# Performance work log

Hardware: AMD Instinct MI355X
Metric: run time of the kernel (lower is better)

## Reference

```python
import jax, jax.numpy as jnp
import numpy as np

B, N, C = 8, 1024, 1024
H = 16
D = C // H  # head_dim = 64


def apply_rope(t, cos, sin):
    # t: (B,H,N,D), cos/sin: (N, D//2). Interleaved-pair RoPE
    # (matches repeat_interleave(2) + stack(-y2,y1) in the torch code).
    tr = t.reshape(*t.shape[:-1], D // 2, 2)
    t1, t2 = tr[..., 0], tr[..., 1]
    o1 = t1 * cos - t2 * sin
    o2 = t2 * cos + t1 * sin
    return jnp.stack((o1, o2), axis=-1).reshape(t.shape)


def setup_inputs() -> dict:
    key = jax.random.key(0)
    k1, k2, k3, k4 = jax.random.split(key, 4)
    s = 0.02
    x = jax.random.normal(k1, (B, N, C), dtype=jnp.float32)
    w_qkv = jax.random.normal(k2, (C, 3 * C), dtype=jnp.float32) * s  # qkv_bias=False
    w_proj = jax.random.normal(k3, (C, C), dtype=jnp.float32) * s
    b_proj = jax.random.normal(k4, (C,), dtype=jnp.float32) * s
    return {"x": x, "w_qkv": w_qkv, "w_proj": w_proj, "b_proj": b_proj}


def reference(x, w_qkv, w_proj, b_proj):
    # QKV projection: (B,N,3C) -> (3,B,H,N,D)
    qkv = (x @ w_qkv).reshape(B, N, 3, H, D).transpose(2, 0, 3, 1, 4)
    q, k, v = qkv[0], qkv[1], qkv[2]

    # RoPE tables: pos = arange(N) (mask=None, no cls/registers)
    pos = jnp.arange(N, dtype=jnp.float32)
    omega = 1.0 / (10000.0 ** (jnp.arange(D // 2, dtype=jnp.float32) / (D / 2.0)))
    freq = pos[:, None] * omega  # (N, D//2)
    cos, sin = jnp.cos(freq), jnp.sin(freq)

    q = apply_rope(q, cos, sin)
    k = apply_rope(k, cos, sin)

    # Scaled dot-product attention (non-causal, no dropout in eval)
    scale = 1.0 / jnp.sqrt(jnp.float32(D))
    scores = jnp.einsum('bhqd,bhkd->bhqk', q, k) * scale
    attn = jax.nn.softmax(scores, axis=-1)
    out = jnp.einsum('bhqk,bhkd->bhqd', attn, v)

    # Merge heads + output projection
    out = out.transpose(0, 2, 1, 3).reshape(B, N, C)
    return out @ w_proj + b_proj
```

## Files before the change

kernel.cpp:

```cpp
#include <hip/hip_runtime.h>
#include <hip/hip_bf16.h>
#include <math.h>

#define Bsz  8
#define Nseq 1024
#define Cdim 1024
#define Hh   16
#define Dd   64

typedef short short8 __attribute__((ext_vector_type(8)));
typedef float floatx4 __attribute__((ext_vector_type(4)));

__device__ __forceinline__ unsigned short f2bf(float f) {
    __hip_bfloat16 h = __float2bfloat16(f);
    return __builtin_bit_cast(unsigned short, h);
}

__device__ __forceinline__ void async16(const void* g, void* l) {
    __builtin_amdgcn_global_load_lds(
        (const __attribute__((address_space(1))) unsigned int*)g,
        (__attribute__((address_space(3))) unsigned int*)l, 16, 0, 0);
}

__device__ __forceinline__ unsigned pack_bf16(float lo, float hi) {
    unsigned ulo = __float_as_uint(lo) + 0x8000u;
    unsigned uhi = __float_as_uint(hi) + 0x8000u;
    return __builtin_amdgcn_perm(uhi, ulo, 0x07060302);
}

__global__ __launch_bounds__(256) void prep(
    const float* __restrict__ x, const float* __restrict__ w_qkv,
    const float* __restrict__ w_proj,
    unsigned short* __restrict__ xb, unsigned short* __restrict__ wqkvt,
    unsigned short* __restrict__ wprojt, float2* __restrict__ rope)
{
    __shared__ float T[64][65];
    const int blk = blockIdx.x;
    const int tid = threadIdx.x;

    if (blk < 8192) {
        int i = blk * 256 + tid;
        float4 v = ((const float4*)x)[i];
        ushort4 u;
        u.x = f2bf(v.x); u.y = f2bf(v.y); u.z = f2bf(v.z); u.w = f2bf(v.w);
        ((ushort4*)xb)[i] = u;
        return;
    }
    if (blk < 9216) {
        const float* in;
        unsigned short* out;
        int R = 1024, Ccols, c0, r0;
        if (blk < 8960) {
            int b2 = blk - 8192;
            in = w_qkv; out = wqkvt; Ccols = 3072;
            c0 = (b2 % 48) * 64; r0 = (b2 / 48) * 64;
        } else {
            int b2 = blk - 8960;
            in = w_proj; out = wprojt; Ccols = 1024;
            c0 = (b2 % 16) * 64; r0 = (b2 / 16) * 64;
        }
        for (int i = tid; i < 4096; i += 256) {
            int r = i >> 6, c = i & 63;
            T[r][c] = in[(size_t)(r0 + r) * Ccols + c0 + c];
        }
        __syncthreads();
        for (int i = tid; i < 4096; i += 256) {
            int rr = i >> 6, cc = i & 63;
            out[(size_t)(c0 + rr) * R + r0 + cc] = f2bf(T[cc][rr]);
        }
        return;
    }
    {
        int i = (blk - 9216) * 256 + tid;
        int n = i >> 5, p = i & 31;
        float omega = __expf(-(float)p * 0.2878231366242557f);
        float sv, cv;
        sincosf((float)n * omega, &sv, &cv);
        rope[i] = make_float2(cv, sv);
    }
}

template <int MODE>
__global__ __launch_bounds__(256) void gemm_bf16(
    const unsigned short* __restrict__ A, const unsigned short* __restrict__ Bt,
    const float* __restrict__ bias, const float2* __restrict__ rope,
    unsigned short* __restrict__ qb, unsigned short* __restrict__ kb,
    unsigned short* __restrict__ vtb, float* __restrict__ out)
{
    const int K = 1024;
    __shared__ short SM[2][128][64];
    const int tid  = threadIdx.x;
    const int wave = tid >> 6, lane = tid & 63;
    const int ml = lane & 15, quad = lane >> 4;
    const int wm = wave >> 1, wn = wave & 1;

    int lin = blockIdx.y * gridDim.x + blockIdx.x;
    const int nwg = gridDim.x * gridDim.y;
    lin = (lin & 7) * (nwg >> 3) + (lin >> 3);
    const int bx = lin % gridDim.x, by = lin / gridDim.x;
    const int bm = by * 128, bn = bx * 128;

    const int lr     = lane >> 3;
    const int lchunk = ((lane & 7) ^ lr) * 8;

    floatx4 acc[4][4] = {};

    for (int k0 = 0; k0 < K; k0 += 64) {
        #pragma unroll
        for (int t = 0; t < 4; ++t) {
            int r8  = (wave * 4 + t) * 8;
            int row = r8 + lr;
            async16(A  + (size_t)(bm + row) * K + k0 + lchunk, &SM[0][r8][0]);
            async16(Bt + (size_t)(bn + row) * K + k0 + lchunk, &SM[1][r8][0]);
        }
        __syncthreads();

        #pragma unroll
        for (int ks = 0; ks < 2; ++ks) {
            const int sl = ((ks * 4 + quad) ^ (ml & 7)) * 8;
            short8 araw[4], braw[4];
            #pragma unroll
            for (int mi = 0; mi < 4; ++mi)
                araw[mi] = *(const short8*)&SM[0][wm * 64 + mi * 16 + ml][sl];
            #pragma unroll
            for (int ni = 0; ni < 4; ++ni)
                braw[ni] = *(const short8*)&SM[1][wn * 64 + ni * 16 + ml][sl];
            #pragma unroll
            for (int mi = 0; mi < 4; ++mi)
                #pragma unroll
                for (int ni = 0; ni < 4; ++ni)
                    acc[mi][ni] = __builtin_amdgcn_mfma_f32_16x16x32_bf16(
                        araw[mi], braw[ni], acc[mi][ni], 0, 0, 0);
        }
        __syncthreads();
    }

    if (MODE == 0) {
        const int region = bn >> 10;
        const int b = bm >> 10;
        if (region < 2) {
            float2* Rs = (float2*)&SM[0][0][0];
            #pragma unroll
            for (int t = 0; t < 16; ++t) {
                int idx = t * 256 + tid;
                Rs[idx] = rope[(size_t)((bm + (idx >> 5)) & 1023) * 32 + (idx & 31)];
            }
            __syncthreads();
            unsigned short* dst = (region == 0) ? qb : kb;
            const float scale = (region == 0) ? 0.125f : 1.f;
            const float sgn = (ml & 1) ? 1.f : -1.f;
            #pragma unroll
            for (int ni = 0; ni < 4; ++ni) {
                int col = bn + wn * 64 + ni * 16 + ml;
                int jj = col & 1023;
                int h = jj >> 6, d = jj & 63;
                int p = d >> 1;
                #pragma unroll
                for (int mi = 0; mi < 4; ++mi)
                    #pragma unroll
                    for (int r = 0; r < 4; ++r) {
                        int rl = wm * 64 + mi * 16 + quad * 4 + r;
                        int n  = (bm + rl) & 1023;
                        float val = acc[mi][ni][r];
                        float partner = __shfl_xor(val, 1);
                        float2 cs = Rs[rl * 32 + p];
                        dst[(((size_t)(b * Hh + h)) * Nseq + n) * Dd + d] =
                            f2bf((val * cs.x + sgn * partner * cs.y) * scale);
                    }
            }
        } else {
            short* T = &SM[0][0][0];
            const int n0 = bm & 1023;
            #pragma unroll
            for (int hw = 0; hw < 2; ++hw) {
                if (hw) __syncthreads();
                if (wn == hw) {
                    #pragma unroll
                    for (int ni = 0; ni < 4; ++ni) {
                        int dcol = ni * 16 + ml;
                        #pragma unroll
                        for (int mi = 0; mi < 4; ++mi)
                            #pragma unroll
                            for (int r = 0; r < 4; ++r) {
                                int rl = wm * 64 + mi * 16 + quad * 4 + r;
                                T[dcol * 132 + rl] = (short)f2bf(acc[mi][ni][r]);
                            }
                    }
                }
                __syncthreads();
                int h = ((bn & 1023) >> 6) + hw;
                #pragma unroll
                for (int t = 0; t < 8; ++t) {
                    int idx4 = t * 256 + tid;
                    int d = idx4 >> 5, seg = idx4 & 31;
                    ushort4 v4 = *(const ushort4*)&T[d * 132 + seg * 4];
                    *(ushort4*)(vtb + (((size_t)(b * Hh + h)) * Dd + d) * Nseq
                                + n0 + seg * 4) = v4;
                }
            }
        }
    } else {
        #pragma unroll
        for (int ni = 0; ni < 4; ++ni) {
            int col = bn + wn * 64 + ni * 16 + ml;
            float bv = bias[col];
            #pragma unroll
            for (int mi = 0; mi < 4; ++mi)
                #pragma unroll
                for (int r = 0; r < 4; ++r) {
                    int row = bm + wm * 64 + mi * 16 + quad * 4 + r;
                    out[(size_t)row * 1024 + col] = acc[mi][ni][r] + bv;
                }
        }
    }
}

__global__ __launch_bounds__(256, 4) void attn_flash_mfma(
    const unsigned short* __restrict__ qb, const unsigned short* __restrict__ kb,
    const unsigned short* __restrict__ vt, unsigned short* __restrict__ ao)
{
    const int bh  = blockIdx.x;
    const int qt  = blockIdx.y;
    const int tid = threadIdx.x;
    const int wave = tid >> 6, lane = tid & 63;
    const int ml = lane & 15, quad = lane >> 4;
    const int lr = lane >> 3;
    const int lc = ((lane & 7) ^ lr) * 8;

    __shared__ __attribute__((aligned(16))) short SMEM[17408];
    short (*Ks)[64] = (short(*)[64])SMEM;
    short* U = SMEM + 4096;
    short (*Qs)[64] = (short(*)[64])U;
    short (*Vs)[64] = (short(*)[64])U;
    short (*Ps)[32][72] = (short(*)[32][72])(U + 4096);

    const size_t hbase = (size_t)bh * (Nseq * Dd);
    const size_t vbase = (size_t)bh * 64;
    const int q0 = qt * 128;
    const int wq = wave * 32;
    const int wk = wave * 16;

    #pragma unroll
    for (int t = 0; t < 4; ++t)
        async16(qb + hbase + (size_t)(q0 + wq + t * 8 + lr) * 64 + lc, &Qs[wq + t * 8][0]);
    async16(kb + hbase + (size_t)(wk + lr) * 64 + lc,     &Ks[wk][0]);
    async16(kb + hbase + (size_t)(wk + 8 + lr) * 64 + lc, &Ks[wk + 8][0]);
    __syncthreads();

    short8 qfr[2][2];
    #pragma unroll
    for (int ks = 0; ks < 2; ++ks) {
        const int sl = ((ks * 4 + quad) ^ (ml & 7)) * 8;
        qfr[ks][0] = *(const short8*)&Qs[wq + ml][sl];
        qfr[ks][1] = *(const short8*)&Qs[wq + 16 + ml][sl];
    }
    __syncthreads();

    float l0 = 0.f, l1 = 0.f;
    floatx4 o[2][4] = {};

    for (int kt = 0; kt < 16; ++kt) {
        const int k0r = kt * 64;
        async16(vt + (vbase + wk + lr) * Nseq + k0r + lc,     &Vs[wk][0]);
        async16(vt + (vbase + wk + 8 + lr) * Nseq + k0r + lc, &Vs[wk + 8][0]);

        floatx4 st[2][4] = {};
        __builtin_amdgcn_s_setprio(1);
        #pragma unroll
        for (int ks = 0; ks < 2; ++ks) {
            const int sl = ((ks * 4 + quad) ^ (ml & 7)) * 8;
            #pragma unroll
            for (int kbk = 0; kbk < 4; ++kbk) {
                short8 kf = *(const short8*)&Ks[kbk * 16 + ml][sl];
                st[0][kbk] = __builtin_amdgcn_mfma_f32_16x16x32_bf16(kf, qfr[ks][0], st[0][kbk], 0, 0, 0);
                st[1][kbk] = __builtin_amdgcn_mfma_f32_16x16x32_bf16(kf, qfr[ks][1], st[1][kbk], 0, 0, 0);
            }
        }
        __builtin_amdgcn_s_setprio(0);

        #pragma unroll
        for (int qg = 0; qg < 2; ++qg) {
            float lacc = 0.f;
            #pragma unroll
            for (int kbk = 0; kbk < 4; ++kbk) {
                float e0 = __expf(st[qg][kbk][0]);
                float e1 = __expf(st[qg][kbk][1]);
                float e2 = __expf(st[qg][kbk][2]);
                float e3 = __expf(st[qg][kbk][3]);
                lacc += (e0 + e1) + (e2 + e3);
                uint2 pk;
                pk.x = pack_bf16(e0, e1);
                pk.y = pack_bf16(e2, e3);
                *(uint2*)&Ps[wave][qg * 16 + ml][kbk * 16 + quad * 4] = pk;
            }
            if (qg == 0) l0 += lacc; else l1 += lacc;
        }
        __syncthreads();

        if (kt < 15) {
            const int k1r = k0r + 64;
            async16(kb + hbase + (size_t)(k1r + wk + lr) * 64 + lc,     &Ks[wk][0]);
            async16(kb + hbase + (size_t)(k1r + wk + 8 + lr) * 64 + lc, &Ks[wk + 8][0]);
        }

        __builtin_amdgcn_s_setprio(1);
        #pragma unroll
        for (int ks = 0; ks < 2; ++ks) {
            const int sl = ((ks * 4 + quad) ^ (ml & 7)) * 8;
            short8 pf0 = *(const short8*)&Ps[wave][ml][ks * 32 + quad * 8];
            short8 pf1 = *(const short8*)&Ps[wave][16 + ml][ks * 32 + quad * 8];
            #pragma unroll
            for (int nt = 0; nt < 4; ++nt) {
                short8 vf = *(const short8*)&Vs[nt * 16 + ml][sl];
                o[0][nt] = __builtin_amdgcn_mfma_f32_16x16x32_bf16(pf0, vf, o[0][nt], 0, 0, 0);
                o[1][nt] = __builtin_amdgcn_mfma_f32_16x16x32_bf16(pf1, vf, o[1][nt], 0, 0, 0);
            }
        }
        __builtin_amdgcn_s_setprio(0);
        if (kt < 15)
            __syncthreads();
    }

    l0 += __shfl_xor(l0, 16);
    l0 += __shfl_xor(l0, 32);
    l1 += __shfl_xor(l1, 16);
    l1 += __shfl_xor(l1, 32);

    const int b = bh >> 4, h = bh & 15;
    #pragma unroll
    for (int qg = 0; qg < 2; ++qg) {
        float lsrc = (qg == 0) ? l0 : l1;
        #pragma unroll
        for (int r = 0; r < 4; ++r) {
            float lq = __shfl(lsrc, quad * 4 + r);
            float inv = 1.f / lq;
            int q = q0 + wq + qg * 16 + quad * 4 + r;
            size_t rowbase = ((size_t)(b * Nseq + q)) * Cdim + h * Dd;
            #pragma unroll
            for (int nt = 0; nt < 4; ++nt)
                ao[rowbase + nt * 16 + ml] = f2bf(o[qg][nt][r] * inv);
        }
    }
}

extern "C" void kernel_launch(void* const* d_in, const int* in_sizes, int n_in,
                              void* d_out, int out_size, void* d_ws, size_t ws_size,
                              hipStream_t stream) {
    const float* x      = (const float*)d_in[0];
    const float* w_qkv  = (const float*)d_in[1];
    const float* w_proj = (const float*)d_in[2];
    const float* b_proj = (const float*)d_in[3];
    float* out = (float*)d_out;

    const size_t M8 = (size_t)8 * 1024 * 1024;
    unsigned short* qb     = (unsigned short*)d_ws;
    unsigned short* kb     = qb + M8;
    unsigned short* vt     = kb + M8;
    unsigned short* xb     = vt + M8;
    unsigned short* wqkvt  = xb + M8;
    unsigned short* wprojt = wqkvt + 3 * 1024 * 1024;
    float2*         rope   = (float2*)(wprojt + 1024 * 1024);
    unsigned short* aob    = xb;

    prep<<<9344, 256, 0, stream>>>(x, w_qkv, w_proj, xb, wqkvt, wprojt, rope);

    gemm_bf16<0><<<dim3(24, 64), 256, 0, stream>>>(xb, wqkvt, nullptr, rope,
                                                   qb, kb, vt, nullptr);

    attn_flash_mfma<<<dim3(128, 8), 256, 0, stream>>>(qb, kb, vt, aob);

    gemm_bf16<1><<<dim3(8, 64), 256, 0, stream>>>(aob, wprojt, b_proj, nullptr,
                                                  nullptr, nullptr, nullptr, out);
}
```

Before: 232.0 us.

## Rewrite QKV GEMM as 256x256-tile, 8-wave kernel with pipelined async LDS staging

Replaces the templated 128x128 QKV GEMM with a dedicated 256x256-tile kernel of 512 threads. It stages K in 32-wide halves into double-buffered, swizzled LDS via global_load_lds, and uses explicit vmcnt waits, barriers and s_setprio around the MFMA clusters. The goal is to overlap global-to-LDS copies with matrix math and raise per-block reuse for the largest GEMM. The cost is 128KB of LDS per block and heavy register use, which limits occupancy. The V-transpose epilogue also gets packed stores.

```diff
diff --git a/kernel.cpp b/kernel.cpp
--- a/kernel.cpp
+++ b/kernel.cpp
@@ -80,12 +80,176 @@
     }
 }
 
-template <int MODE>
-__global__ __launch_bounds__(256) void gemm_bf16(
+#define AH(b,k) (((b)*2+(k))*8192)
+#define BH(b,k) (32768+((b)*2+(k))*8192)
+
+__device__ __forceinline__ void stage_half(const unsigned short* g, int kbase,
+                                           short* dst, int wave, int lane) {
+    #pragma unroll
+    for (int inst = 0; inst < 2; ++inst) {
+        int sb = (inst * 8 + wave) * 64;
+        int slot = sb + lane;
+        int p = slot >> 3, sp = (slot & 7) ^ (p & 7);
+        int grow = p * 2 + (sp >> 2);
+        int gcol = kbase + (sp & 3) * 8;
+        async16(g + (size_t)grow * 1024 + gcol, dst + sb * 8);
+    }
+}
+
+__device__ __forceinline__ void ld4(short8 d[4], const short* hb, int rbase,
+                                    int ml, int quad) {
+    #pragma unroll
+    for (int f = 0; f < 4; ++f) {
+        int row = rbase + f * 16 + ml;
+        int p = row >> 1;
+        int sl = (((row & 1) << 2) | quad) ^ (p & 7);
+        d[f] = *(const short8*)&hb[p * 64 + sl * 8];
+    }
+}
+
+__device__ __forceinline__ void mma16(floatx4 acc[8][4], int mb,
+                                      const short8 ar[4], const short8 br[4]) {
+    #pragma unroll
+    for (int f = 0; f < 4; ++f)
+        #pragma unroll
+        for (int n = 0; n < 4; ++n)
+            acc[mb + f][n] = __builtin_amdgcn_mfma_f32_16x16x32_bf16(
+                ar[f], br[n], acc[mb + f][n], 0, 0, 0);
+}
+
+#define VMW4 asm volatile("s_waitcnt vmcnt(4)" ::: "memory")
+#define VMW0 asm volatile("s_waitcnt vmcnt(0)" ::: "memory")
+#define BARA do { __builtin_amdgcn_s_barrier();                          \
+                  asm volatile("s_waitcnt lgkmcnt(0)" ::: "memory");     \
+                  __builtin_amdgcn_sched_barrier(0); } while (0)
+#define BARB __builtin_amdgcn_s_barrier()
+
+#define KT(T, S12, S34, WAITX) {                                          \
+    const int bu = (T) & 1, nb = bu ^ 1;                                  \
+                                                      \
+    ld4(ar, SM + AH(bu,0), wm * 128,      ml, quad);                      \
+    ld4(br, SM + BH(bu,0), wn * 64,       ml, quad);                      \
+    if (S12) stage_half(Agp, ((T)+1)*64 + 32, SM + AH(nb,1), wave, lane); \
+    BARA; __builtin_amdgcn_s_setprio(1); mma16(acc, 0, ar, br);           \
+    __builtin_amdgcn_s_setprio(0); BARB;                                  \
+                                 \
+    ld4(ar, SM + AH(bu,0), wm * 128 + 64, ml, quad);                      \
+    if (S12) stage_half(Bgp, ((T)+1)*64 + 32, SM + BH(nb,1), wave, lane); \
+    BARA; __builtin_amdgcn_s_setprio(1); mma16(acc, 4, ar, br);           \
+    __builtin_amdgcn_s_setprio(0); BARB;                                  \
+                                                      \
+    ld4(ar, SM + AH(bu,1), wm * 128,      ml, quad);                      \
+    ld4(br, SM + BH(bu,1), wn * 64,       ml, quad);                      \
+    if (S34) stage_half(Agp, ((T)+2)*64,      SM + AH(bu,0), wave, lane); \
+    BARA; __builtin_amdgcn_s_setprio(1); mma16(acc, 0, ar, br);           \
+    __builtin_amdgcn_s_setprio(0); BARB;                                  \
+                                                      \
+    ld4(ar, SM + AH(bu,1), wm * 128 + 64, ml, quad);                      \
+    if (S34) stage_half(Bgp, ((T)+2)*64,      SM + BH(bu,0), wave, lane); \
+    WAITX;                                                                \
+    BARA; __builtin_amdgcn_s_setprio(1); mma16(acc, 4, ar, br);           \
+    __builtin_amdgcn_s_setprio(0); BARB;                                  \
+}
+
+__global__ __launch_bounds__(512, 2) void gemm_qkv(
     const unsigned short* __restrict__ A, const unsigned short* __restrict__ Bt,
-    const float* __restrict__ bias, const float2* __restrict__ rope,
+    const float2* __restrict__ rope,
     unsigned short* __restrict__ qb, unsigned short* __restrict__ kb,
-    unsigned short* __restrict__ vtb, float* __restrict__ out)
+    unsigned short* __restrict__ vtb)
+{
+    __shared__ __attribute__((aligned(16))) short SM[65536];
+    const int tid  = threadIdx.x;
+    const int wave = tid >> 6, lane = tid & 63;
+    const int ml = lane & 15, quad = lane >> 4;
+    const int wm = wave >> 2, wn = wave & 3;
+
+    int lin = blockIdx.y * 12 + blockIdx.x;
+    lin = (lin & 7) * 48 + (lin >> 3);
+    const int bm = (lin / 12) * 256, bn = (lin % 12) * 256;
+
+    const unsigned short* Agp = A  + (size_t)bm * 1024;
+    const unsigned short* Bgp = Bt + (size_t)bn * 1024;
+
+    floatx4 acc[8][4] = {};
+    short8 ar[4], br[4];
+
+    stage_half(Agp,  0, SM + AH(0,0), wave, lane);
+    stage_half(Bgp,  0, SM + BH(0,0), wave, lane);
+    stage_half(Agp, 32, SM + AH(0,1), wave, lane);
+    stage_half(Bgp, 32, SM + BH(0,1), wave, lane);
+    stage_half(Agp, 64, SM + AH(1,0), wave, lane);
+    stage_half(Bgp, 64, SM + BH(1,0), wave, lane);
+    VMW4;
+    BARB;
+
+    KT(0, 1, 1, VMW4)  KT(1, 1, 1, VMW4)  KT(2, 1, 1, VMW4)  KT(3, 1, 1, VMW4)
+    KT(4, 1, 1, VMW4)  KT(5, 1, 1, VMW4)  KT(6, 1, 1, VMW4)  KT(7, 1, 1, VMW4)
+    KT(8, 1, 1, VMW4)  KT(9, 1, 1, VMW4)  KT(10, 1, 1, VMW4) KT(11, 1, 1, VMW4)
+    KT(12, 1, 1, VMW4) KT(13, 1, 1, VMW4) KT(14, 1, 0, VMW0) KT(15, 0, 0, (void)0)
+
+    const int region = bn >> 10;
+    const int b  = bm >> 10;
+    const int n0 = bm & 1023;
+    if (region < 2) {
+        float2* Rs = (float2*)SM;
+        for (int i = tid; i < 8192; i += 512)
+            Rs[i] = rope[(size_t)(n0 + (i >> 5)) * 32 + (i & 31)];
+        __syncthreads();
+        unsigned short* dst = (region == 0) ? qb : kb;
+        const float scale = (region == 0) ? 0.125f : 1.f;
+        const float sgn = (ml & 1) ? 1.f : -1.f;
+        #pragma unroll
+        for (int ni = 0; ni < 4; ++ni) {
+            int jj = (bn & 1023) + wn * 64 + ni * 16 + ml;
+            int h = jj >> 6, d = jj & 63, pp = d >> 1;
+            #pragma unroll
+            for (int mi = 0; mi < 8; ++mi)
+                #pragma unroll
+                for (int r = 0; r < 4; ++r) {
+                    int rl = wm * 128 + mi * 16 + quad * 4 + r;
+                    float val = acc[mi][ni][r];
+                    float partner = __shfl_xor(val, 1);
+                    float2 cs = Rs[rl * 32 + pp];
+                    dst[(((size_t)(b * Hh + h)) * Nseq + n0 + rl) * Dd + d] =
+                        f2bf((val * cs.x + sgn * partner * cs.y) * scale);
+                }
+        }
+    } else {
+        short* T = SM;
+        const int hb = (bn & 1023) >> 6;
+        #pragma unroll
+        for (int hw = 0; hw < 2; ++hw) {
+            if (hw) __syncthreads();
+            if (wm == hw) {
+                #pragma unroll
+                for (int ni = 0; ni < 4; ++ni) {
+                    int c = wn * 64 + ni * 16 + ml;
+                    #pragma unroll
+                    for (int mi = 0; mi < 8; ++mi) {
+                        uint2 pk;
+                        pk.x = pack_bf16(acc[mi][ni][0], acc[mi][ni][1]);
+                        pk.y = pack_bf16(acc[mi][ni][2], acc[mi][ni][3]);
+                        *(uint2*)&T[c * 136 + mi * 16 + quad * 4] = pk;
+                    }
+                }
+            }
+            __syncthreads();
+            #pragma unroll
+            for (int i = 0; i < 16; ++i) {
+                int idx = i * 512 + tid;
+                int c = idx >> 5, seg = idx & 31;
+                ushort4 v4 = *(const ushort4*)&T[c * 136 + seg * 4];
+                int h = hb + (c >> 6), d = c & 63;
+                *(ushort4*)(vtb + (((size_t)(b * Hh + h)) * Dd + d) * Nseq
+                            + n0 + hw * 128 + seg * 4) = v4;
+            }
+        }
+    }
+}
+
+__global__ __launch_bounds__(256) void gemm_proj(
+    const unsigned short* __restrict__ A, const unsigned short* __restrict__ Bt,
+    const float* __restrict__ bias, float* __restrict__ out)
 {
     const int K = 1024;
     __shared__ short SM[2][128][64];
@@ -135,83 +299,17 @@
         __syncthreads();
     }
 
-    if (MODE == 0) {
-        const int region = bn >> 10;
-        const int b = bm >> 10;
-        if (region < 2) {
-            float2* Rs = (float2*)&SM[0][0][0];
-            #pragma unroll
-            for (int t = 0; t < 16; ++t) {
-                int idx = t * 256 + tid;
-                Rs[idx] = rope[(size_t)((bm + (idx >> 5)) & 1023) * 32 + (idx & 31)];
-            }
-            __syncthreads();
-            unsigned short* dst = (region == 0) ? qb : kb;
-            const float scale = (region == 0) ? 0.125f : 1.f;
-            const float sgn = (ml & 1) ? 1.f : -1.f;
-            #pragma unroll
-            for (int ni = 0; ni < 4; ++ni) {
-                int col = bn + wn * 64 + ni * 16 + ml;
-                int jj = col & 1023;
-                int h = jj >> 6, d = jj & 63;
-                int p = d >> 1;
-                #pragma unroll
-                for (int mi = 0; mi < 4; ++mi)
-                    #pragma unroll
-                    for (int r = 0; r < 4; ++r) {
-                        int rl = wm * 64 + mi * 16 + quad * 4 + r;
-                        int n  = (bm + rl) & 1023;
-                        float val = acc[mi][ni][r];
-                        float partner = __shfl_xor(val, 1);
-                        float2 cs = Rs[rl * 32 + p];
-                        dst[(((size_t)(b * Hh + h)) * Nseq + n) * Dd + d] =
-                            f2bf((val * cs.x + sgn * partner * cs.y) * scale);
-                    }
-            }
-        } else {
-            short* T = &SM[0][0][0];
-            const int n0 = bm & 1023;
-            #pragma unroll
-            for (int hw = 0; hw < 2; ++hw) {
-                if (hw) __syncthreads();
-                if (wn == hw) {
-                    #pragma unroll
-                    for (int ni = 0; ni < 4; ++ni) {
-                        int dcol = ni * 16 + ml;
-                        #pragma unroll
-                        for (int mi = 0; mi < 4; ++mi)
-                            #pragma unroll
-                            for (int r = 0; r < 4; ++r) {
-                                int rl = wm * 64 + mi * 16 + quad * 4 + r;
-                                T[dcol * 132 + rl] = (short)f2bf(acc[mi][ni][r]);
-                            }
-                    }
-                }
-                __syncthreads();
-                int h = ((bn & 1023) >> 6) + hw;
-                #pragma unroll
-                for (int t = 0; t < 8; ++t) {
-                    int idx4 = t * 256 + tid;
-                    int d = idx4 >> 5, seg = idx4 & 31;
-                    ushort4 v4 = *(const ushort4*)&T[d * 132 + seg * 4];
-                    *(ushort4*)(vtb + (((size_t)(b * Hh + h)) * Dd + d) * Nseq
-                                + n0 + seg * 4) = v4;
-                }
-            }
-        }
-    } else {
-        #pragma unroll
-        for (int ni = 0; ni < 4; ++ni) {
-            int col = bn + wn * 64 + ni * 16 + ml;
-            float bv = bias[col];
-            #pragma unroll
-            for (int mi = 0; mi < 4; ++mi)
-                #pragma unroll
-                for (int r = 0; r < 4; ++r) {
-                    int row = bm + wm * 64 + mi * 16 + quad * 4 + r;
-                    out[(size_t)row * 1024 + col] = acc[mi][ni][r] + bv;
-                }
-        }
+    #pragma unroll
+    for (int ni = 0; ni < 4; ++ni) {
+        int col = bn + wn * 64 + ni * 16 + ml;
+        float bv = bias[col];
+        #pragma unroll
+        for (int mi = 0; mi < 4; ++mi)
+            #pragma unroll
+            for (int r = 0; r < 4; ++r) {
+                int row = bm + wm * 64 + mi * 16 + quad * 4 + r;
+                out[(size_t)row * 1024 + col] = acc[mi][ni][r] + bv;
+            }
     }
 }
 
@@ -364,11 +462,9 @@
 
     prep<<<9344, 256, 0, stream>>>(x, w_qkv, w_proj, xb, wqkvt, wprojt, rope);
 
-    gemm_bf16<0><<<dim3(24, 64), 256, 0, stream>>>(xb, wqkvt, nullptr, rope,
-                                                   qb, kb, vt, nullptr);
+    gemm_qkv<<<dim3(12, 32), 512, 0, stream>>>(xb, wqkvt, rope, qb, kb, vt);
 
     attn_flash_mfma<<<dim3(128, 8), 256, 0, stream>>>(qb, kb, vt, aob);
 
-    gemm_bf16<1><<<dim3(8, 64), 256, 0, stream>>>(aob, wprojt, b_proj, nullptr,
-                                                  nullptr, nullptr, nullptr, out);
-}
+    gemm_proj<<<dim3(8, 64), 256, 0, stream>>>(aob, wprojt, b_proj, out);
+}
```

Measured after the change: 237.0 us. +2.2%, slower.

## Double-buffer K/V tiles in flash attention and drop mid-iteration barrier

Applied to the files above, without the earlier changes.

Keeps two LDS buffers each for K and V and prefetches the next key tile into the idle buffer at the start of each iteration, so global loads overlap the QK and PV MFMA work. The block-wide barrier between the softmax write and the PV step becomes a wave-local lgkmcnt wait, since each wave only reads its own P tile, leaving one barrier per iteration. LDS use grows from about 34 KB to 50 KB per block and the occupancy hint drops from 4 to 3 blocks, which may reduce latency hiding.

```diff
diff --git a/kernel.cpp b/kernel.cpp
--- a/kernel.cpp
+++ b/kernel.cpp
@@ -215,7 +215,7 @@
     }
 }
 
-__global__ __launch_bounds__(256, 4) void attn_flash_mfma(
+__global__ __launch_bounds__(256, 3) void attn_flash_mfma(
     const unsigned short* __restrict__ qb, const unsigned short* __restrict__ kb,
     const unsigned short* __restrict__ vt, unsigned short* __restrict__ ao)
 {
@@ -227,24 +227,27 @@
     const int lr = lane >> 3;
     const int lc = ((lane & 7) ^ lr) * 8;
 
-    __shared__ __attribute__((aligned(16))) short SMEM[17408];
-    short (*Ks)[64] = (short(*)[64])SMEM;
-    short* U = SMEM + 4096;
-    short (*Qs)[64] = (short(*)[64])U;
-    short (*Vs)[64] = (short(*)[64])U;
-    short (*Ps)[32][72] = (short(*)[32][72])(U + 4096);
+    __shared__ __attribute__((aligned(16))) short SMEM[25600];
+    short* const KsB = SMEM;
+    short* const VsB = SMEM + 8192;
+    short (*Qs)[64] = (short(*)[64])(SMEM + 16384);
+    short* const PsB = SMEM + 16384;
+    const int psw = 16384 + wave * 2304;
 
     const size_t hbase = (size_t)bh * (Nseq * Dd);
     const size_t vbase = (size_t)bh * 64;
     const int q0 = qt * 128;
     const int wq = wave * 32;
     const int wk = wave * 16;
+    (void)PsB;
 
     #pragma unroll
     for (int t = 0; t < 4; ++t)
         async16(qb + hbase + (size_t)(q0 + wq + t * 8 + lr) * 64 + lc, &Qs[wq + t * 8][0]);
-    async16(kb + hbase + (size_t)(wk + lr) * 64 + lc,     &Ks[wk][0]);
-    async16(kb + hbase + (size_t)(wk + 8 + lr) * 64 + lc, &Ks[wk + 8][0]);
+    async16(kb + hbase + (size_t)(wk + lr) * 64 + lc,     KsB + (wk)     * 64);
+    async16(kb + hbase + (size_t)(wk + 8 + lr) * 64 + lc, KsB + (wk + 8) * 64);
+    async16(vt + (vbase + wk + lr) * Nseq + lc,           VsB + (wk)     * 64);
+    async16(vt + (vbase + wk + 8 + lr) * Nseq + lc,       VsB + (wk + 8) * 64);
     __syncthreads();
 
     short8 qfr[2][2];
@@ -260,9 +263,19 @@
     floatx4 o[2][4] = {};
 
     for (int kt = 0; kt < 16; ++kt) {
-        const int k0r = kt * 64;
-        async16(vt + (vbase + wk + lr) * Nseq + k0r + lc,     &Vs[wk][0]);
-        async16(vt + (vbase + wk + 8 + lr) * Nseq + k0r + lc, &Vs[wk + 8][0]);
+        const int bu = kt & 1;
+        const short* Kb = KsB + bu * 4096;
+        const short* Vb = VsB + bu * 4096;
+
+        if (kt < 15) {
+            const int k1r = (kt + 1) * 64;
+            short* Kn = KsB + (bu ^ 1) * 4096;
+            short* Vn = VsB + (bu ^ 1) * 4096;
+            async16(kb + hbase + (size_t)(k1r + wk + lr) * 64 + lc,     Kn + (wk)     * 64);
+            async16(kb + hbase + (size_t)(k1r + wk + 8 + lr) * 64 + lc, Kn + (wk + 8) * 64);
+            async16(vt + (vbase + wk + lr) * Nseq + k1r + lc,           Vn + (wk)     * 64);
+            async16(vt + (vbase + wk + 8 + lr) * Nseq + k1r + lc,       Vn + (wk + 8) * 64);
+        }
 
         floatx4 st[2][4] = {};
         __builtin_amdgcn_s_setprio(1);
@@ -271,7 +284,7 @@
             const int sl = ((ks * 4 + quad) ^ (ml & 7)) * 8;
             #pragma unroll
             for (int kbk = 0; kbk < 4; ++kbk) {
-                short8 kf = *(const short8*)&Ks[kbk * 16 + ml][sl];
+                short8 kf = *(const short8*)&Kb[(kbk * 16 + ml) * 64 + sl];
                 st[0][kbk] = __builtin_amdgcn_mfma_f32_16x16x32_bf16(kf, qfr[ks][0], st[0][kbk], 0, 0, 0);
                 st[1][kbk] = __builtin_amdgcn_mfma_f32_16x16x32_bf16(kf, qfr[ks][1], st[1][kbk], 0, 0, 0);
             }
@@ -291,34 +304,32 @@
                 uint2 pk;
                 pk.x = pack_bf16(e0, e1);
                 pk.y = pack_bf16(e2, e3);
-                *(uint2*)&Ps[wave][qg * 16 + ml][kbk * 16 + quad * 4] = pk;
+                *(uint2*)&SMEM[psw + (qg * 16 + ml) * 72 + kbk * 16 + quad * 4] = pk;
             }
             if (qg == 0) l0 += lacc; else l1 += lacc;
         }
-        __syncthreads();
-
-        if (kt < 15) {
-            const int k1r = k0r + 64;
-            async16(kb + hbase + (size_t)(k1r + wk + lr) * 64 + lc,     &Ks[wk][0]);
-            async16(kb + hbase + (size_t)(k1r + wk + 8 + lr) * 64 + lc, &Ks[wk + 8][0]);
-        }
+        asm volatile("s_waitcnt lgkmcnt(0)" ::: "memory");
+        __builtin_amdgcn_sched_barrier(0);
 
         __builtin_amdgcn_s_setprio(1);
         #pragma unroll
         for (int ks = 0; ks < 2; ++ks) {
             const int sl = ((ks * 4 + quad) ^ (ml & 7)) * 8;
-            short8 pf0 = *(const short8*)&Ps[wave][ml][ks * 32 + quad * 8];
-            short8 pf1 = *(const short8*)&Ps[wave][16 + ml][ks * 32 + quad * 8];
+            short8 pf0 = *(const short8*)&SMEM[psw + (ml) * 72 + ks * 32 + quad * 8];
+            short8 pf1 = *(const short8*)&SMEM[psw + (16 + ml) * 72 + ks * 32 + quad * 8];
             #pragma unroll
             for (int nt = 0; nt < 4; ++nt) {
-                short8 vf = *(const short8*)&Vs[nt * 16 + ml][sl];
+                short8 vf = *(const short8*)&Vb[(nt * 16 + ml) * 64 + sl];
                 o[0][nt] = __builtin_amdgcn_mfma_f32_16x16x32_bf16(pf0, vf, o[0][nt], 0, 0, 0);
                 o[1][nt] = __builtin_amdgcn_mfma_f32_16x16x32_bf16(pf1, vf, o[1][nt], 0, 0, 0);
             }
         }
         __builtin_amdgcn_s_setprio(0);
-        if (kt < 15)
-            __syncthreads();
+
+        if (kt < 15) {
+            asm volatile("s_waitcnt vmcnt(0)" ::: "memory");
+            __builtin_amdgcn_s_barrier();
+        }
     }
 
     l0 += __shfl_xor(l0, 16);
```

New measurement: 239.8 us. 1.03x slower.

## Fuse Q/K/V column tiles into one QKV GEMM block and use raw exp2

Applied to the files above, without the earlier changes.

The QKV projection becomes a dedicated kernel in which each block computes the Q, K and V tiles for the same 128 columns, so every A tile loaded into shared memory is reused three times. This needs 3x the accumulators and 64KB of LDS, with launch bounds set for 2 blocks per CU. The q scale is folded with log2(e), which lets attention call the raw v_exp_f32 instruction instead of __expf and drops the multiply inside exp. The risks are lower occupancy and register pressure from the 192-float accumulator, plus reduced pipelining because the load loop is single-buffered.

```diff
diff --git a/kernel.cpp b/kernel.cpp
--- a/kernel.cpp
+++ b/kernel.cpp
@@ -26,6 +26,12 @@
     unsigned ulo = __float_as_uint(lo) + 0x8000u;
     unsigned uhi = __float_as_uint(hi) + 0x8000u;
     return __builtin_amdgcn_perm(uhi, ulo, 0x07060302);
+}
+
+__device__ __forceinline__ float exp2_raw(float x) {
+    float r;
+    asm("v_exp_f32 %0, %1" : "=v"(r) : "v"(x));
+    return r;
 }
 
 __global__ __launch_bounds__(256) void prep(
@@ -80,12 +86,138 @@
     }
 }
 
-template <int MODE>
-__global__ __launch_bounds__(256) void gemm_bf16(
+__global__ __launch_bounds__(256, 2) void gemm_qkv(
     const unsigned short* __restrict__ A, const unsigned short* __restrict__ Bt,
-    const float* __restrict__ bias, const float2* __restrict__ rope,
+    const float2* __restrict__ rope,
     unsigned short* __restrict__ qb, unsigned short* __restrict__ kb,
-    unsigned short* __restrict__ vtb, float* __restrict__ out)
+    unsigned short* __restrict__ vtb)
+{
+    __shared__ __attribute__((aligned(16))) short SM[32768];
+    const int tid  = threadIdx.x;
+    const int wave = tid >> 6, lane = tid & 63;
+    const int ml = lane & 15, quad = lane >> 4;
+    const int wm = wave >> 1, wn = wave & 1;
+
+    int lin = blockIdx.y * 8 + blockIdx.x;
+    lin = (lin & 7) * 64 + (lin >> 3);
+    const int bm = (lin >> 3) * 128;
+    const int bn = (lin & 7) * 128;
+
+    const int lr     = lane >> 3;
+    const int lchunk = ((lane & 7) ^ lr) * 8;
+
+    floatx4 acc[3][4][4] = {};
+
+    for (int k0 = 0; k0 < 1024; k0 += 64) {
+        #pragma unroll
+        for (int t = 0; t < 4; ++t) {
+            int r8 = (wave * 4 + t) * 8;
+            async16(A + (size_t)(bm + r8 + lr) * 1024 + k0 + lchunk, &SM[r8 * 64]);
+        }
+        #pragma unroll
+        for (int rg = 0; rg < 3; ++rg)
+            #pragma unroll
+            for (int t = 0; t < 4; ++t) {
+                int r8 = (wave * 4 + t) * 8;
+                async16(Bt + (size_t)(rg * 1024 + bn + r8 + lr) * 1024 + k0 + lchunk,
+                        &SM[8192 + rg * 8192 + r8 * 64]);
+            }
+        __syncthreads();
+
+        #pragma unroll
+        for (int ks = 0; ks < 2; ++ks) {
+            const int sl = ((ks * 4 + quad) ^ (ml & 7)) * 8;
+            short8 araw[4];
+            #pragma unroll
+            for (int mi = 0; mi < 4; ++mi)
+                araw[mi] = *(const short8*)&SM[(wm * 64 + mi * 16 + ml) * 64 + sl];
+            #pragma unroll
+            for (int rg = 0; rg < 3; ++rg) {
+                short8 braw[4];
+                #pragma unroll
+                for (int ni = 0; ni < 4; ++ni)
+                    braw[ni] = *(const short8*)&SM[8192 + rg * 8192 +
+                                                   (wn * 64 + ni * 16 + ml) * 64 + sl];
+                #pragma unroll
+                for (int mi = 0; mi < 4; ++mi)
+                    #pragma unroll
+                    for (int ni = 0; ni < 4; ++ni)
+                        acc[rg][mi][ni] = __builtin_amdgcn_mfma_f32_16x16x32_bf16(
+                            araw[mi], braw[ni], acc[rg][mi][ni], 0, 0, 0);
+            }
+        }
+        __syncthreads();
+    }
+
+    const int b  = bm >> 10;
+    const int n0 = bm & 1023;
+
+    float2* Rs = (float2*)SM;
+    #pragma unroll
+    for (int t = 0; t < 16; ++t) {
+        int idx = t * 256 + tid;
+        Rs[idx] = rope[(size_t)(n0 + (idx >> 5)) * 32 + (idx & 31)];
+    }
+    __syncthreads();
+
+    #pragma unroll
+    for (int rg = 0; rg < 2; ++rg) {
+        unsigned short* dst = (rg == 0) ? qb : kb;
+        const float scale = (rg == 0) ? 0.1803368801111602f : 1.f;
+        const float sgn = (ml & 1) ? 1.f : -1.f;
+        #pragma unroll
+        for (int ni = 0; ni < 4; ++ni) {
+            int jj = bn + wn * 64 + ni * 16 + ml;
+            int h = jj >> 6, d = jj & 63, p = d >> 1;
+            #pragma unroll
+            for (int mi = 0; mi < 4; ++mi)
+                #pragma unroll
+                for (int r = 0; r < 4; ++r) {
+                    int rl = wm * 64 + mi * 16 + quad * 4 + r;
+                    float val = acc[rg][mi][ni][r];
+                    float partner = __shfl_xor(val, 1);
+                    float2 cs = Rs[rl * 32 + p];
+                    dst[(((size_t)(b * Hh + h)) * Nseq + n0 + rl) * Dd + d] =
+                        f2bf((val * cs.x + sgn * partner * cs.y) * scale);
+                }
+        }
+    }
+
+    {
+        short* T = SM + 16384;
+        #pragma unroll
+        for (int hw = 0; hw < 2; ++hw) {
+            if (hw) __syncthreads();
+            if (wn == hw) {
+                #pragma unroll
+                for (int ni = 0; ni < 4; ++ni) {
+                    int dcol = ni * 16 + ml;
+                    #pragma unroll
+                    for (int mi = 0; mi < 4; ++mi)
+                        #pragma unroll
+                        for (int r = 0; r < 4; ++r) {
+                            int rl = wm * 64 + mi * 16 + quad * 4 + r;
+                            T[dcol * 132 + rl] = (short)f2bf(acc[2][mi][ni][r]);
+                        }
+                }
+            }
+            __syncthreads();
+            int h = (bn >> 6) + hw;
+            #pragma unroll
+            for (int t = 0; t < 8; ++t) {
+                int idx4 = t * 256 + tid;
+                int d = idx4 >> 5, seg = idx4 & 31;
+                ushort4 v4 = *(const ushort4*)&T[d * 132 + seg * 4];
+                *(ushort4*)(vtb + (((size_t)(b * Hh + h)) * Dd + d) * Nseq
+                            + n0 + seg * 4) = v4;
+            }
+        }
+    }
+}
+
+__global__ __launch_bounds__(256) void gemm_proj(
+    const unsigned short* __restrict__ A, const unsigned short* __restrict__ Bt,
+    const float* __restrict__ bias, float* __restrict__ out)
 {
     const int K = 1024;
     __shared__ short SM[2][128][64];
@@ -135,83 +267,17 @@
         __syncthreads();
     }
 
-    if (MODE == 0) {
-        const int region = bn >> 10;
-        const int b = bm >> 10;
-        if (region < 2) {
-            float2* Rs = (float2*)&SM[0][0][0];
-            #pragma unroll
-            for (int t = 0; t < 16; ++t) {
-                int idx = t * 256 + tid;
-                Rs[idx] = rope[(size_t)((bm + (idx >> 5)) & 1023) * 32 + (idx & 31)];
-            }
-            __syncthreads();
-            unsigned short* dst = (region == 0) ? qb : kb;
-            const float scale = (region == 0) ? 0.125f : 1.f;
-            const float sgn = (ml & 1) ? 1.f : -1.f;
-            #pragma unroll
-            for (int ni = 0; ni < 4; ++ni) {
-                int col = bn + wn * 64 + ni * 16 + ml;
-                int jj = col & 1023;
-                int h = jj >> 6, d = jj & 63;
-                int p = d >> 1;
-                #pragma unroll
-                for (int mi = 0; mi < 4; ++mi)
-                    #pragma unroll
-                    for (int r = 0; r < 4; ++r) {
-                        int rl = wm * 64 + mi * 16 + quad * 4 + r;
-                        int n  = (bm + rl) & 1023;
-                        float val = acc[mi][ni][r];
-                        float partner = __shfl_xor(val, 1);
-                        float2 cs = Rs[rl * 32 + p];
-                        dst[(((size_t)(b * Hh + h)) * Nseq + n) * Dd + d] =
-                            f2bf((val * cs.x + sgn * partner * cs.y) * scale);
-                    }
-            }
-        } else {
-            short* T = &SM[0][0][0];
-            const int n0 = bm & 1023;
-            #pragma unroll
-            for (int hw = 0; hw < 2; ++hw) {
-                if (hw) __syncthreads();
-                if (wn == hw) {
-                    #pragma unroll
-                    for (int ni = 0; ni < 4; ++ni) {
-                        int dcol = ni * 16 + ml;
-                        #pragma unroll
-                        for (int mi = 0; mi < 4; ++mi)
-                            #pragma unroll
-                            for (int r = 0; r < 4; ++r) {
-                                int rl = wm * 64 + mi * 16 + quad * 4 + r;
-                                T[dcol * 132 + rl] = (short)f2bf(acc[mi][ni][r]);
-                            }
-                    }
-                }
-                __syncthreads();
-                int h = ((bn & 1023) >> 6) + hw;
-                #pragma unroll
-                for (int t = 0; t < 8; ++t) {
-                    int idx4 = t * 256 + tid;
-                    int d = idx4 >> 5, seg = idx4 & 31;
-                    ushort4 v4 = *(const ushort4*)&T[d * 132 + seg * 4];
-                    *(ushort4*)(vtb + (((size_t)(b * Hh + h)) * Dd + d) * Nseq
-                                + n0 + seg * 4) = v4;
-                }
-            }
-        }
-    } else {
-        #pragma unroll
-        for (int ni = 0; ni < 4; ++ni) {
-            int col = bn + wn * 64 + ni * 16 + ml;
-            float bv = bias[col];
-            #pragma unroll
-            for (int mi = 0; mi < 4; ++mi)
-                #pragma unroll
-                for (int r = 0; r < 4; ++r) {
-                    int row = bm + wm * 64 + mi * 16 + quad * 4 + r;
-                    out[(size_t)row * 1024 + col] = acc[mi][ni][r] + bv;
-                }
-        }
+    #pragma unroll
+    for (int ni = 0; ni < 4; ++ni) {
+        int col = bn + wn * 64 + ni * 16 + ml;
+        float bv = bias[col];
+        #pragma unroll
+        for (int mi = 0; mi < 4; ++mi)
+            #pragma unroll
+            for (int r = 0; r < 4; ++r) {
+                int row = bm + wm * 64 + mi * 16 + quad * 4 + r;
+                out[(size_t)row * 1024 + col] = acc[mi][ni][r] + bv;
+            }
     }
 }
 
@@ -283,10 +349,10 @@
             float lacc = 0.f;
             #pragma unroll
             for (int kbk = 0; kbk < 4; ++kbk) {
-                float e0 = __expf(st[qg][kbk][0]);
-                float e1 = __expf(st[qg][kbk][1]);
-                float e2 = __expf(st[qg][kbk][2]);
-                float e3 = __expf(st[qg][kbk][3]);
+                float e0 = exp2_raw(st[qg][kbk][0]);
+                float e1 = exp2_raw(st[qg][kbk][1]);
+                float e2 = exp2_raw(st[qg][kbk][2]);
+                float e3 = exp2_raw(st[qg][kbk][3]);
                 lacc += (e0 + e1) + (e2 + e3);
                 uint2 pk;
                 pk.x = pack_bf16(e0, e1);
@@ -364,11 +430,9 @@
 
     prep<<<9344, 256, 0, stream>>>(x, w_qkv, w_proj, xb, wqkvt, wprojt, rope);
 
-    gemm_bf16<0><<<dim3(24, 64), 256, 0, stream>>>(xb, wqkvt, nullptr, rope,
-                                                   qb, kb, vt, nullptr);
+    gemm_qkv<<<dim3(8, 64), 256, 0, stream>>>(xb, wqkvt, rope, qb, kb, vt);
 
     attn_flash_mfma<<<dim3(128, 8), 256, 0, stream>>>(qb, kb, vt, aob);
 
-    gemm_bf16<1><<<dim3(8, 64), 256, 0, stream>>>(aob, wprojt, b_proj, nullptr,
-                                                  nullptr, nullptr, nullptr, out);
-}
+    gemm_proj<<<dim3(8, 64), 256, 0, stream>>>(aob, wprojt, b_proj, out);
+}
```

Measured after the change: 246.7 us. 1.06x slower.
